# Kernel tuning notes

Hardware: AMD Instinct MI355X
Metric: run time of the kernel (lower is better)

The kernel has to match this reference:

```python
import jax, jax.numpy as jnp
import numpy as np

Q_SIZE, K_SIZE, H = 256, 256, 128
N, n, m, D_V = 4, 512, 512, 256

def setup_inputs() -> dict:
    key = jax.random.key(0)
    k1, k2, k3, k4, k5, k6 = jax.random.split(key, 6)
    return {
        "query": jax.random.normal(k1, (N, n, Q_SIZE), dtype=jnp.float32),
        "key": jax.random.normal(k2, (N, m, K_SIZE), dtype=jnp.float32),
        "value": jax.random.normal(k3, (N, m, D_V), dtype=jnp.float32),
        "W_q": jax.random.normal(k4, (Q_SIZE, H), dtype=jnp.float32) / np.sqrt(Q_SIZE),
        "W_k": jax.random.normal(k5, (K_SIZE, H), dtype=jnp.float32) / np.sqrt(K_SIZE),
        "W_v": jax.random.normal(k6, (H,), dtype=jnp.float32) / np.sqrt(H),
    }

def reference(query, key, value, W_q, W_k, W_v):
    q = query @ W_q                      # (N, n, h)
    k = key @ W_k                        # (N, m, h)
    # broadcast additive scores: tanh((N,n,1,h) + (N,1,m,h)) reduced by W_v -> (N,n,m)
    feats = jnp.tanh(q[:, :, None, :] + k[:, None, :, :])
    scores = jnp.einsum('bnmh,h->bnm', feats, W_v)
    attn = jax.nn.softmax(scores, axis=-1)  # softmax over keys m
    return jnp.einsum('bnm,bmd->bnd', attn, value)
```

## Files before the change

kernel.cpp:

```cpp
#include <hip/hip_runtime.h>
#include <math.h>

#define NB   4
#define SEQN 512
#define SEQM 512
#define QS   256
#define HH   128
#define DV   256

static constexpr float kPreScale = 2.8853900817779268f;
static constexpr float kLog2e    = 1.4426950408889634f;

#if __has_builtin(__builtin_amdgcn_exp2f)
__device__ __forceinline__ float fexp2(float x) { return __builtin_amdgcn_exp2f(x); }
#else
__device__ __forceinline__ float fexp2(float x) { return exp2f(x); }
#endif

#if __has_builtin(__builtin_amdgcn_rcpf)
__device__ __forceinline__ float frcp(float x) { return __builtin_amdgcn_rcpf(x); }
#else
__device__ __forceinline__ float frcp(float x) { return 1.0f / x; }
#endif

__global__ __launch_bounds__(256) void proj_kernel(
    const float* __restrict__ query, const float* __restrict__ key,
    const float* __restrict__ Wq, const float* __restrict__ Wk,
    const float* __restrict__ wv,
    float* __restrict__ qt, float* __restrict__ kt) {
  __shared__ float in_lds[8][QS];
  const int t = threadIdx.x;
  const int half = (NB * SEQN) / 8;
  const bool isK = blockIdx.x >= half;
  const int rb   = isK ? (blockIdx.x - half) : blockIdx.x;
  const float* __restrict__ in = isK ? key : query;
  const float* __restrict__ W  = isK ? Wk  : Wq;
  float* __restrict__ outp     = isK ? kt  : qt;
  const int row0 = rb * 8;

  const float4* src = reinterpret_cast<const float4*>(in + (size_t)row0 * QS);
  float4* dst = reinterpret_cast<float4*>(&in_lds[0][0]);
  dst[t] = src[t];
  dst[t + 256] = src[t + 256];
  __syncthreads();

  const int j  = t & 127;
  const int r0 = (t >> 7) * 4;
  float a0 = 0.f, a1 = 0.f, a2 = 0.f, a3 = 0.f;
  for (int k0 = 0; k0 < QS; k0 += 4) {
    const float w0 = W[(k0 + 0) * HH + j];
    const float w1 = W[(k0 + 1) * HH + j];
    const float w2 = W[(k0 + 2) * HH + j];
    const float w3 = W[(k0 + 3) * HH + j];
    const float4 x0 = *reinterpret_cast<const float4*>(&in_lds[r0 + 0][k0]);
    const float4 x1 = *reinterpret_cast<const float4*>(&in_lds[r0 + 1][k0]);
    const float4 x2 = *reinterpret_cast<const float4*>(&in_lds[r0 + 2][k0]);
    const float4 x3 = *reinterpret_cast<const float4*>(&in_lds[r0 + 3][k0]);
    a0 = fmaf(x0.x, w0, fmaf(x0.y, w1, fmaf(x0.z, w2, fmaf(x0.w, w3, a0))));
    a1 = fmaf(x1.x, w0, fmaf(x1.y, w1, fmaf(x1.z, w2, fmaf(x1.w, w3, a1))));
    a2 = fmaf(x2.x, w0, fmaf(x2.y, w1, fmaf(x2.z, w2, fmaf(x2.w, w3, a2))));
    a3 = fmaf(x3.x, w0, fmaf(x3.y, w1, fmaf(x3.z, w2, fmaf(x3.w, w3, a3))));
  }
  const float wvj = wv[j];
  float acc[4] = {a0, a1, a2, a3};
#pragma unroll
  for (int r = 0; r < 4; ++r) {
    const float e  = fexp2(acc[r] * kPreScale);
    const float rc = frcp(e + 1.0f);
    float A = fmaf(-2.0f, rc, 1.0f);
    A = fminf(fmaxf(A, -0.99999988f), 0.99999988f);
    const size_t rowoff = (size_t)(row0 + r0 + r) * (2 * HH);
    outp[rowoff + j]      = A;
    outp[rowoff + HH + j] = wvj * A;
  }
}

__global__ __launch_bounds__(256) void scores_kernel(
    const float* __restrict__ qt, const float* __restrict__ kt,
    float* __restrict__ sc) {
  const int t   = threadIdx.x;
  const int bid = blockIdx.x;
  const int mh  = bid & 1;
  const int nb  = (bid >> 1) & 63;
  const int b   = bid >> 7;
  const int n0  = nb * 8;
  const int m   = mh * 256 + t;

  const float* __restrict__ qrow = qt + ((size_t)b * SEQN + n0) * (2 * HH);
  const float* __restrict__ krow = kt + ((size_t)b * SEQM + m) * (2 * HH);

  float N[8], D[8];
#pragma unroll
  for (int n = 0; n < 8; ++n) { N[n] = 0.f; D[n] = 1.f; }

  for (int h0 = 0; h0 < HH; h0 += 8) {
    const float4 b0 = *reinterpret_cast<const float4*>(krow + h0);
    const float4 b1 = *reinterpret_cast<const float4*>(krow + h0 + 4);
    const float4 u0 = *reinterpret_cast<const float4*>(krow + HH + h0);
    const float4 u1 = *reinterpret_cast<const float4*>(krow + HH + h0 + 4);
#pragma unroll
    for (int n = 0; n < 8; ++n) {
      const float* qr = qrow + (size_t)n * (2 * HH);
      const float4 a0 = *reinterpret_cast<const float4*>(qr + h0);
      const float4 a1 = *reinterpret_cast<const float4*>(qr + h0 + 4);
      const float4 v0 = *reinterpret_cast<const float4*>(qr + HH + h0);
      const float4 v1 = *reinterpret_cast<const float4*>(qr + HH + h0 + 4);
      const float s0 = v0.x + u0.x, d0 = fmaf(a0.x, b0.x, 1.0f);
      const float s1 = v0.y + u0.y, d1 = fmaf(a0.y, b0.y, 1.0f);
      const float s2 = v0.z + u0.z, d2 = fmaf(a0.z, b0.z, 1.0f);
      const float s3 = v0.w + u0.w, d3 = fmaf(a0.w, b0.w, 1.0f);
      const float s4 = v1.x + u1.x, d4 = fmaf(a1.x, b1.x, 1.0f);
      const float s5 = v1.y + u1.y, d5 = fmaf(a1.y, b1.y, 1.0f);
      const float s6 = v1.z + u1.z, d6 = fmaf(a1.z, b1.z, 1.0f);
      const float s7 = v1.w + u1.w, d7 = fmaf(a1.w, b1.w, 1.0f);
      const float t01 = fmaf(s0, d1, s1 * d0), e01 = d0 * d1;
      const float t23 = fmaf(s2, d3, s3 * d2), e23 = d2 * d3;
      const float t45 = fmaf(s4, d5, s5 * d4), e45 = d4 * d5;
      const float t67 = fmaf(s6, d7, s7 * d6), e67 = d6 * d7;
      const float t03 = fmaf(t01, e23, t23 * e01), e03 = e01 * e23;
      const float t47 = fmaf(t45, e67, t67 * e45), e47 = e45 * e67;
      const float t07 = fmaf(t03, e47, t47 * e03), e07 = e03 * e47;
      N[n] = fmaf(N[n], e07, t07 * D[n]);
      D[n] *= e07;
    }
  }
  float* srow = sc + ((size_t)b * SEQN + n0) * SEQM + m;
#pragma unroll
  for (int n = 0; n < 8; ++n)
    srow[(size_t)n * SEQM] = N[n] * frcp(D[n]);
}

__global__ __launch_bounds__(512) void softpv_kernel(
    const float* __restrict__ sc, const float* __restrict__ value,
    float* __restrict__ out) {
  __shared__ float sp[8][SEQM];
  __shared__ float pvbuf[8][8][DV];
  __shared__ float rs[8];

  const int t    = threadIdx.x;
  const int b    = blockIdx.x >> 6;
  const int n0   = (blockIdx.x & 63) * 8;
  const int wave = t >> 6;
  const int lane = t & 63;

  {
    const float* __restrict__ srow = sc + ((size_t)b * SEQN + n0 + wave) * SEQM;
    float v[8];
    float mx = -1e30f;
#pragma unroll
    for (int i = 0; i < 8; ++i) {
      v[i] = srow[lane + 64 * i];
      mx = fmaxf(mx, v[i]);
    }
#pragma unroll
    for (int off = 32; off > 0; off >>= 1) mx = fmaxf(mx, __shfl_xor(mx, off));
    float sum = 0.f;
#pragma unroll
    for (int i = 0; i < 8; ++i) {
      const float p = fexp2((v[i] - mx) * kLog2e);
      sum += p;
      sp[wave][lane + 64 * i] = p;
    }
#pragma unroll
    for (int off = 32; off > 0; off >>= 1) sum += __shfl_xor(sum, off);
    if (lane == 0) rs[wave] = 1.0f / sum;
  }
  __syncthreads();

  const float* __restrict__ vb = value + (size_t)b * SEQM * DV;
  const int dg = t & 63;
  const int mg = t >> 6;
  float oA[8], oB[8], oC[8], oD[8];
#pragma unroll
  for (int n = 0; n < 8; ++n) { oA[n] = 0.f; oB[n] = 0.f; oC[n] = 0.f; oD[n] = 0.f; }
  const int mbeg = mg * 64;
  for (int m0 = mbeg; m0 < mbeg + 64; m0 += 4) {
    float vA[4], vB[4], vC[4], vD[4];
#pragma unroll
    for (int mm = 0; mm < 4; ++mm) {
      const float* vr = vb + (size_t)(m0 + mm) * DV + dg;
      vA[mm] = vr[0];
      vB[mm] = vr[64];
      vC[mm] = vr[128];
      vD[mm] = vr[192];
    }
#pragma unroll
    for (int n = 0; n < 8; ++n) {
      const float4 p4 = *reinterpret_cast<const float4*>(&sp[n][m0]);
      oA[n] = fmaf(p4.x, vA[0], fmaf(p4.y, vA[1], fmaf(p4.z, vA[2], fmaf(p4.w, vA[3], oA[n]))));
      oB[n] = fmaf(p4.x, vB[0], fmaf(p4.y, vB[1], fmaf(p4.z, vB[2], fmaf(p4.w, vB[3], oB[n]))));
      oC[n] = fmaf(p4.x, vC[0], fmaf(p4.y, vC[1], fmaf(p4.z, vC[2], fmaf(p4.w, vC[3], oC[n]))));
      oD[n] = fmaf(p4.x, vD[0], fmaf(p4.y, vD[1], fmaf(p4.z, vD[2], fmaf(p4.w, vD[3], oD[n]))));
    }
  }
#pragma unroll
  for (int n = 0; n < 8; ++n) {
    pvbuf[mg][n][dg]       = oA[n];
    pvbuf[mg][n][dg + 64]  = oB[n];
    pvbuf[mg][n][dg + 128] = oC[n];
    pvbuf[mg][n][dg + 192] = oD[n];
  }
  __syncthreads();

  {
    const int n = wave;
    const float r = rs[n];
    const size_t ob = ((size_t)b * SEQN + n0 + n) * DV;
#pragma unroll
    for (int k = 0; k < 4; ++k) {
      const int d = lane + 64 * k;
      float acc = 0.f;
#pragma unroll
      for (int g = 0; g < 8; ++g) acc += pvbuf[g][n][d];
      out[ob + d] = acc * r;
    }
  }
}

extern "C" void kernel_launch(void* const* d_in, const int* in_sizes, int n_in,
                              void* d_out, int out_size, void* d_ws, size_t ws_size,
                              hipStream_t stream) {
  const float* query = (const float*)d_in[0];
  const float* key   = (const float*)d_in[1];
  const float* value = (const float*)d_in[2];
  const float* W_q   = (const float*)d_in[3];
  const float* W_k   = (const float*)d_in[4];
  const float* W_v   = (const float*)d_in[5];
  float* out = (float*)d_out;

  float* qt = (float*)d_out;
  float* kt = (float*)d_ws;
  float* sc = kt + (size_t)NB * SEQM * (2 * HH);

  proj_kernel<<<2 * (NB * SEQN) / 8, 256, 0, stream>>>(query, key, W_q, W_k, W_v, qt, kt);
  scores_kernel<<<NB * (SEQN / 8) * 2, 256, 0, stream>>>(qt, kt, sc);
  softpv_kernel<<<NB * (SEQN / 8), 512, 0, stream>>>(sc, value, out);
}
```

Before: 53.64 us.

## Fuse score, softmax and PV kernels and transpose key projection layout

Merges the scores kernel and the softmax/PV kernel into one kernel. Each 512-thread block computes the scores for 4 query rows across all 512 keys into LDS, then runs softmax and the value product, so the scores buffer no longer round-trips through global memory and one launch is dropped. The key projection is now stored h-major as interleaved (A, wv*A) float2 pairs, so per-key reads are coalesced across threads. The projection kernel also drops its LDS staging and reads inputs straight from global memory. In exchange, each block holds fewer query rows, which lowers reuse of the key data, and the blocks need more LDS and registers.

```diff
diff --git a/kernel.cpp b/kernel.cpp
--- a/kernel.cpp
+++ b/kernel.cpp
@@ -7,6 +7,7 @@
 #define QS   256
 #define HH   128
 #define DV   256
+#define BM   (NB * SEQM)
 
 static constexpr float kPreScale = 2.8853900817779268f;
 static constexpr float kLog2e    = 1.4426950408889634f;
@@ -27,35 +28,33 @@
     const float* __restrict__ query, const float* __restrict__ key,
     const float* __restrict__ Wq, const float* __restrict__ Wk,
     const float* __restrict__ wv,
-    float* __restrict__ qt, float* __restrict__ kt) {
-  __shared__ float in_lds[8][QS];
+    float* __restrict__ qt, float2* __restrict__ kt) {
   const int t = threadIdx.x;
   const int half = (NB * SEQN) / 8;
   const bool isK = blockIdx.x >= half;
   const int rb   = isK ? (blockIdx.x - half) : blockIdx.x;
   const float* __restrict__ in = isK ? key : query;
   const float* __restrict__ W  = isK ? Wk  : Wq;
-  float* __restrict__ outp     = isK ? kt  : qt;
   const int row0 = rb * 8;
 
-  const float4* src = reinterpret_cast<const float4*>(in + (size_t)row0 * QS);
-  float4* dst = reinterpret_cast<float4*>(&in_lds[0][0]);
-  dst[t] = src[t];
-  dst[t + 256] = src[t + 256];
-  __syncthreads();
-
   const int j  = t & 127;
-  const int r0 = (t >> 7) * 4;
+  const int r0 = __builtin_amdgcn_readfirstlane((t >> 7) * 4);
+
+  const float* __restrict__ x0p = in + (size_t)(row0 + r0 + 0) * QS;
+  const float* __restrict__ x1p = in + (size_t)(row0 + r0 + 1) * QS;
+  const float* __restrict__ x2p = in + (size_t)(row0 + r0 + 2) * QS;
+  const float* __restrict__ x3p = in + (size_t)(row0 + r0 + 3) * QS;
+
   float a0 = 0.f, a1 = 0.f, a2 = 0.f, a3 = 0.f;
   for (int k0 = 0; k0 < QS; k0 += 4) {
     const float w0 = W[(k0 + 0) * HH + j];
     const float w1 = W[(k0 + 1) * HH + j];
     const float w2 = W[(k0 + 2) * HH + j];
     const float w3 = W[(k0 + 3) * HH + j];
-    const float4 x0 = *reinterpret_cast<const float4*>(&in_lds[r0 + 0][k0]);
-    const float4 x1 = *reinterpret_cast<const float4*>(&in_lds[r0 + 1][k0]);
-    const float4 x2 = *reinterpret_cast<const float4*>(&in_lds[r0 + 2][k0]);
-    const float4 x3 = *reinterpret_cast<const float4*>(&in_lds[r0 + 3][k0]);
+    const float4 x0 = *reinterpret_cast<const float4*>(x0p + k0);
+    const float4 x1 = *reinterpret_cast<const float4*>(x1p + k0);
+    const float4 x2 = *reinterpret_cast<const float4*>(x2p + k0);
+    const float4 x3 = *reinterpret_cast<const float4*>(x3p + k0);
     a0 = fmaf(x0.x, w0, fmaf(x0.y, w1, fmaf(x0.z, w2, fmaf(x0.w, w3, a0))));
     a1 = fmaf(x1.x, w0, fmaf(x1.y, w1, fmaf(x1.z, w2, fmaf(x1.w, w3, a1))));
     a2 = fmaf(x2.x, w0, fmaf(x2.y, w1, fmaf(x2.z, w2, fmaf(x2.w, w3, a2))));
@@ -69,50 +68,57 @@
     const float rc = frcp(e + 1.0f);
     float A = fmaf(-2.0f, rc, 1.0f);
     A = fminf(fmaxf(A, -0.99999988f), 0.99999988f);
-    const size_t rowoff = (size_t)(row0 + r0 + r) * (2 * HH);
-    outp[rowoff + j]      = A;
-    outp[rowoff + HH + j] = wvj * A;
+    const int grow = row0 + r0 + r;
+    if (isK) {
+      kt[(size_t)j * BM + grow] = make_float2(A, wvj * A);
+    } else {
+      qt[(size_t)grow * (2 * HH) + j]      = A;
+      qt[(size_t)grow * (2 * HH) + HH + j] = wvj * A;
+    }
   }
 }
 
-__global__ __launch_bounds__(256) void scores_kernel(
-    const float* __restrict__ qt, const float* __restrict__ kt,
-    float* __restrict__ sc) {
-  const int t   = threadIdx.x;
-  const int bid = blockIdx.x;
-  const int mh  = bid & 1;
-  const int nb  = (bid >> 1) & 63;
-  const int b   = bid >> 7;
-  const int n0  = nb * 8;
-  const int m   = mh * 256 + t;
-
-  const float* __restrict__ qrow = qt + ((size_t)b * SEQN + n0) * (2 * HH);
-  const float* __restrict__ krow = kt + ((size_t)b * SEQM + m) * (2 * HH);
-
-  float N[8], D[8];
-#pragma unroll
-  for (int n = 0; n < 8; ++n) { N[n] = 0.f; D[n] = 1.f; }
+__global__ __launch_bounds__(512) void fused_kernel(
+    const float* __restrict__ qt, const float2* __restrict__ kt,
+    const float* __restrict__ value, float* __restrict__ out) {
+  __shared__ float sp[4][SEQM];
+  __shared__ float pvbuf[8][4][DV];
+  __shared__ float wred[16];
+
+  const int t  = threadIdx.x;
+  const int b  = blockIdx.x >> 7;
+  const int n0 = (blockIdx.x & 127) * 4;
+  const int m  = t;
+
+  const float* __restrict__ qb = qt + ((size_t)b * SEQN + n0) * (2 * HH);
+  const float2* __restrict__ kb = kt + (size_t)b * SEQM + m;
+
+  float N[4], D[4];
+#pragma unroll
+  for (int n = 0; n < 4; ++n) { N[n] = 0.f; D[n] = 1.f; }
 
   for (int h0 = 0; h0 < HH; h0 += 8) {
-    const float4 b0 = *reinterpret_cast<const float4*>(krow + h0);
-    const float4 b1 = *reinterpret_cast<const float4*>(krow + h0 + 4);
-    const float4 u0 = *reinterpret_cast<const float4*>(krow + HH + h0);
-    const float4 u1 = *reinterpret_cast<const float4*>(krow + HH + h0 + 4);
-#pragma unroll
-    for (int n = 0; n < 8; ++n) {
-      const float* qr = qrow + (size_t)n * (2 * HH);
+    float kA[8], kW[8];
+#pragma unroll
+    for (int jj = 0; jj < 8; ++jj) {
+      const float2 f = kb[(size_t)(h0 + jj) * BM];
+      kA[jj] = f.x; kW[jj] = f.y;
+    }
+#pragma unroll
+    for (int n = 0; n < 4; ++n) {
+      const float* qr = qb + n * (2 * HH);
       const float4 a0 = *reinterpret_cast<const float4*>(qr + h0);
       const float4 a1 = *reinterpret_cast<const float4*>(qr + h0 + 4);
       const float4 v0 = *reinterpret_cast<const float4*>(qr + HH + h0);
       const float4 v1 = *reinterpret_cast<const float4*>(qr + HH + h0 + 4);
-      const float s0 = v0.x + u0.x, d0 = fmaf(a0.x, b0.x, 1.0f);
-      const float s1 = v0.y + u0.y, d1 = fmaf(a0.y, b0.y, 1.0f);
-      const float s2 = v0.z + u0.z, d2 = fmaf(a0.z, b0.z, 1.0f);
-      const float s3 = v0.w + u0.w, d3 = fmaf(a0.w, b0.w, 1.0f);
-      const float s4 = v1.x + u1.x, d4 = fmaf(a1.x, b1.x, 1.0f);
-      const float s5 = v1.y + u1.y, d5 = fmaf(a1.y, b1.y, 1.0f);
-      const float s6 = v1.z + u1.z, d6 = fmaf(a1.z, b1.z, 1.0f);
-      const float s7 = v1.w + u1.w, d7 = fmaf(a1.w, b1.w, 1.0f);
+      const float s0 = v0.x + kW[0], d0 = fmaf(a0.x, kA[0], 1.0f);
+      const float s1 = v0.y + kW[1], d1 = fmaf(a0.y, kA[1], 1.0f);
+      const float s2 = v0.z + kW[2], d2 = fmaf(a0.z, kA[2], 1.0f);
+      const float s3 = v0.w + kW[3], d3 = fmaf(a0.w, kA[3], 1.0f);
+      const float s4 = v1.x + kW[4], d4 = fmaf(a1.x, kA[4], 1.0f);
+      const float s5 = v1.y + kW[5], d5 = fmaf(a1.y, kA[5], 1.0f);
+      const float s6 = v1.z + kW[6], d6 = fmaf(a1.z, kA[6], 1.0f);
+      const float s7 = v1.w + kW[7], d7 = fmaf(a1.w, kA[7], 1.0f);
       const float t01 = fmaf(s0, d1, s1 * d0), e01 = d0 * d1;
       const float t23 = fmaf(s2, d3, s3 * d2), e23 = d2 * d3;
       const float t45 = fmaf(s4, d5, s5 * d4), e45 = d4 * d5;
@@ -124,95 +130,80 @@
       D[n] *= e07;
     }
   }
-  float* srow = sc + ((size_t)b * SEQN + n0) * SEQM + m;
-#pragma unroll
-  for (int n = 0; n < 8; ++n)
-    srow[(size_t)n * SEQM] = N[n] * frcp(D[n]);
-}
-
-__global__ __launch_bounds__(512) void softpv_kernel(
-    const float* __restrict__ sc, const float* __restrict__ value,
-    float* __restrict__ out) {
-  __shared__ float sp[8][SEQM];
-  __shared__ float pvbuf[8][8][DV];
-  __shared__ float rs[8];
-
-  const int t    = threadIdx.x;
-  const int b    = blockIdx.x >> 6;
-  const int n0   = (blockIdx.x & 63) * 8;
+#pragma unroll
+  for (int n = 0; n < 4; ++n) sp[n][m] = N[n] * frcp(D[n]);
+  __syncthreads();
+
   const int wave = t >> 6;
   const int lane = t & 63;
+  const int row  = wave & 3;
+  const int hv   = wave >> 2;
+  float v[4];
+  float mx = -1e30f;
+#pragma unroll
+  for (int i = 0; i < 4; ++i) {
+    v[i] = sp[row][hv * 256 + lane + 64 * i];
+    mx = fmaxf(mx, v[i]);
+  }
+#pragma unroll
+  for (int off = 32; off > 0; off >>= 1) mx = fmaxf(mx, __shfl_xor(mx, off));
+  if (lane == 0) wred[wave] = mx;
+  __syncthreads();
+  mx = fmaxf(wred[row], wred[row + 4]);
+  float sum = 0.f;
+#pragma unroll
+  for (int i = 0; i < 4; ++i) {
+    const float p = fexp2((v[i] - mx) * kLog2e);
+    sum += p;
+    sp[row][hv * 256 + lane + 64 * i] = p;
+  }
+#pragma unroll
+  for (int off = 32; off > 0; off >>= 1) sum += __shfl_xor(sum, off);
+  if (lane == 0) wred[8 + wave] = sum;
+  __syncthreads();
+
+  const float* __restrict__ vb = value + (size_t)b * SEQM * DV;
+  const int dq = (t & 63) * 4;
+  const int mg = t >> 6;
+  float o[4][4];
+#pragma unroll
+  for (int n = 0; n < 4; ++n)
+#pragma unroll
+    for (int jj = 0; jj < 4; ++jj) o[n][jj] = 0.f;
+  const int mbeg = mg * 64;
+  for (int mi = 0; mi < 64; mi += 4) {
+    const int m0 = mbeg + mi;
+    const float4 vv0 = *reinterpret_cast<const float4*>(vb + (size_t)(m0 + 0) * DV + dq);
+    const float4 vv1 = *reinterpret_cast<const float4*>(vb + (size_t)(m0 + 1) * DV + dq);
+    const float4 vv2 = *reinterpret_cast<const float4*>(vb + (size_t)(m0 + 2) * DV + dq);
+    const float4 vv3 = *reinterpret_cast<const float4*>(vb + (size_t)(m0 + 3) * DV + dq);
+#pragma unroll
+    for (int n = 0; n < 4; ++n) {
+      const float4 p4 = *reinterpret_cast<const float4*>(&sp[n][m0]);
+      o[n][0] = fmaf(p4.x, vv0.x, fmaf(p4.y, vv1.x, fmaf(p4.z, vv2.x, fmaf(p4.w, vv3.x, o[n][0]))));
+      o[n][1] = fmaf(p4.x, vv0.y, fmaf(p4.y, vv1.y, fmaf(p4.z, vv2.y, fmaf(p4.w, vv3.y, o[n][1]))));
+      o[n][2] = fmaf(p4.x, vv0.z, fmaf(p4.y, vv1.z, fmaf(p4.z, vv2.z, fmaf(p4.w, vv3.z, o[n][2]))));
+      o[n][3] = fmaf(p4.x, vv0.w, fmaf(p4.y, vv1.w, fmaf(p4.z, vv2.w, fmaf(p4.w, vv3.w, o[n][3]))));
+    }
+  }
+#pragma unroll
+  for (int n = 0; n < 4; ++n)
+    *reinterpret_cast<float4*>(&pvbuf[mg][n][dq]) =
+        make_float4(o[n][0], o[n][1], o[n][2], o[n][3]);
+  __syncthreads();
 
   {
-    const float* __restrict__ srow = sc + ((size_t)b * SEQN + n0 + wave) * SEQM;
-    float v[8];
-    float mx = -1e30f;
-#pragma unroll
-    for (int i = 0; i < 8; ++i) {
-      v[i] = srow[lane + 64 * i];
-      mx = fmaxf(mx, v[i]);
-    }
-#pragma unroll
-    for (int off = 32; off > 0; off >>= 1) mx = fmaxf(mx, __shfl_xor(mx, off));
-    float sum = 0.f;
-#pragma unroll
-    for (int i = 0; i < 8; ++i) {
-      const float p = fexp2((v[i] - mx) * kLog2e);
-      sum += p;
-      sp[wave][lane + 64 * i] = p;
-    }
-#pragma unroll
-    for (int off = 32; off > 0; off >>= 1) sum += __shfl_xor(sum, off);
-    if (lane == 0) rs[wave] = 1.0f / sum;
-  }
-  __syncthreads();
-
-  const float* __restrict__ vb = value + (size_t)b * SEQM * DV;
-  const int dg = t & 63;
-  const int mg = t >> 6;
-  float oA[8], oB[8], oC[8], oD[8];
-#pragma unroll
-  for (int n = 0; n < 8; ++n) { oA[n] = 0.f; oB[n] = 0.f; oC[n] = 0.f; oD[n] = 0.f; }
-  const int mbeg = mg * 64;
-  for (int m0 = mbeg; m0 < mbeg + 64; m0 += 4) {
-    float vA[4], vB[4], vC[4], vD[4];
-#pragma unroll
-    for (int mm = 0; mm < 4; ++mm) {
-      const float* vr = vb + (size_t)(m0 + mm) * DV + dg;
-      vA[mm] = vr[0];
-      vB[mm] = vr[64];
-      vC[mm] = vr[128];
-      vD[mm] = vr[192];
-    }
-#pragma unroll
-    for (int n = 0; n < 8; ++n) {
-      const float4 p4 = *reinterpret_cast<const float4*>(&sp[n][m0]);
-      oA[n] = fmaf(p4.x, vA[0], fmaf(p4.y, vA[1], fmaf(p4.z, vA[2], fmaf(p4.w, vA[3], oA[n]))));
-      oB[n] = fmaf(p4.x, vB[0], fmaf(p4.y, vB[1], fmaf(p4.z, vB[2], fmaf(p4.w, vB[3], oB[n]))));
-      oC[n] = fmaf(p4.x, vC[0], fmaf(p4.y, vC[1], fmaf(p4.z, vC[2], fmaf(p4.w, vC[3], oC[n]))));
-      oD[n] = fmaf(p4.x, vD[0], fmaf(p4.y, vD[1], fmaf(p4.z, vD[2], fmaf(p4.w, vD[3], oD[n]))));
-    }
-  }
-#pragma unroll
-  for (int n = 0; n < 8; ++n) {
-    pvbuf[mg][n][dg]       = oA[n];
-    pvbuf[mg][n][dg + 64]  = oB[n];
-    pvbuf[mg][n][dg + 128] = oC[n];
-    pvbuf[mg][n][dg + 192] = oD[n];
-  }
-  __syncthreads();
-
-  {
-    const int n = wave;
-    const float r = rs[n];
-    const size_t ob = ((size_t)b * SEQN + n0 + n) * DV;
-#pragma unroll
-    for (int k = 0; k < 4; ++k) {
-      const int d = lane + 64 * k;
+    const int cn    = wave & 3;
+    const int dbase = (wave >> 2) * 128;
+    const float rsn = frcp(wred[8 + cn] + wred[8 + cn + 4]);
+    const size_t ob = ((size_t)b * SEQN + n0 + cn) * DV;
+#pragma unroll
+    for (int k2 = 0; k2 < 2; ++k2) {
+      const int d = dbase + k2 * 64 + lane;
       float acc = 0.f;
 #pragma unroll
-      for (int g = 0; g < 8; ++g) acc += pvbuf[g][n][d];
-      out[ob + d] = acc * r;
+      for (int g = 0; g < 8; ++g) acc += pvbuf[g][cn][d];
+      out[ob + d] = acc * rsn;
     }
   }
 }
@@ -228,11 +219,9 @@
   const float* W_v   = (const float*)d_in[5];
   float* out = (float*)d_out;
 
-  float* qt = (float*)d_out;
-  float* kt = (float*)d_ws;
-  float* sc = kt + (size_t)NB * SEQM * (2 * HH);
+  float*  qt = (float*)d_out;
+  float2* kt = (float2*)d_ws;
 
   proj_kernel<<<2 * (NB * SEQN) / 8, 256, 0, stream>>>(query, key, W_q, W_k, W_v, qt, kt);
-  scores_kernel<<<NB * (SEQN / 8) * 2, 256, 0, stream>>>(qt, kt, sc);
-  softpv_kernel<<<NB * (SEQN / 8), 512, 0, stream>>>(sc, value, out);
+  fused_kernel<<<NB * (SEQN / 4), 512, 0, stream>>>(qt, kt, value, out);
 }
```

New measurement: 52.63 us. About the same (-1.9%).
